# Optimization experiments

Measured on AMD Instinct MI355X. Metric: run time of the kernel, lower is better.

## Reference

```python
import jax, jax.numpy as jnp
import numpy as np

VOCAB, EMBED, HIDDEN = 32000, 256, 512
N, L = 64, 2048

def setup_inputs() -> dict:
    key = jax.random.key(0)
    k1, k2, k3, k4 = jax.random.split(key, 4)
    X = jax.random.randint(k1, (N, L), 0, VOCAB)
    E = jax.random.normal(k2, (VOCAB, EMBED), dtype=jnp.float32) * 0.02
    W_hh = jax.random.normal(k3, (HIDDEN, HIDDEN), dtype=jnp.float32) / np.sqrt(HIDDEN)
    b_hh = jnp.zeros((HIDDEN,), dtype=jnp.float32)
    W_xh = jax.random.normal(k4, (EMBED, HIDDEN), dtype=jnp.float32) / np.sqrt(EMBED)
    b_xh = jnp.zeros((HIDDEN,), dtype=jnp.float32)
    return {"X": X, "E": E, "W_hh": W_hh, "b_hh": b_hh, "W_xh": W_xh, "b_xh": b_xh}

def reference(X, E, W_hh, b_hh, W_xh, b_xh):
    # Embed tokens: (N, L, De)
    xe = E[X]
    # Precompute input projection for all timesteps in one big GEMM: (N, L, H)
    xp = jnp.einsum('nld,dh->nlh', xe, W_xh) + b_xh
    h0 = jnp.zeros((X.shape[0], W_hh.shape[0]), dtype=E.dtype)

    def step(h, x_t):
        # h: (N, H); x_t: (N, H) already projected
        h_new = jnp.tanh(h @ W_hh + b_hh + x_t)
        return h_new, None

    # scan over time: move L to leading axis -> (L, N, H)
    h_last, _ = jax.lax.scan(step, h0, jnp.swapaxes(xp, 0, 1))
    return h_last
```

## Files before the change

kernel.cpp:

```cpp
#include <hip/hip_runtime.h>

typedef _Float16 h8 __attribute__((ext_vector_type(8)));
typedef float f4v __attribute__((ext_vector_type(4)));
typedef unsigned int u32;
typedef unsigned short u16;
typedef unsigned long long u64;
typedef u32 u32x4 __attribute__((ext_vector_type(4)));

#define SEQ 2048
#define HID 512
#define EMB 256
#define NV 32000
#define LOSCALE 2048.0f
#define INV_LOSCALE 4.8828125e-4f

#define WS_WHI 0u
#define WS_WLO (512u * 1024u)
#define WS_HG (1024u * 1024u)
#define WS_FLAGS (WS_HG + 256u * 1024u)
#define WS_PROJ (WS_FLAGS + 4u * 1024u)

__global__ void wsplit_kernel(const float* __restrict__ Whh,
                              _Float16* __restrict__ Whi,
                              _Float16* __restrict__ Wlo) {
  int gid = blockIdx.x * 256 + threadIdx.x;
  int l = gid & 63, c = gid >> 6;
  int kb = c & 15, jtg = c >> 4;
  int j = jtg * 16 + (l & 15);
  int k0 = kb * 32 + (l >> 4) * 8;
  _Float16 hi[8], lo[8];
#pragma unroll
  for (int e = 0; e < 8; ++e) {
    float v = Whh[(k0 + e) * HID + j];
    _Float16 h = (_Float16)v;
    hi[e] = h;
    lo[e] = (_Float16)((v - (float)h) * LOSCALE);
  }
  *(h8*)(Whi + (size_t)gid * 8) = *(const h8*)hi;
  *(h8*)(Wlo + (size_t)gid * 8) = *(const h8*)lo;
}

template <bool PF32>
__global__ __launch_bounds__(256) void proj_kernel(const float* __restrict__ E,
                                                   const float* __restrict__ Wxh,
                                                   const float* __restrict__ bxh,
                                                   void* __restrict__ projE) {
  __shared__ float El[32 * EMB];
  const int t = threadIdx.x;
  const int v0 = blockIdx.x * 32;
  {
    const float4* src = (const float4*)(E + (size_t)v0 * EMB);
    float4* dst = (float4*)El;
#pragma unroll
    for (int i = 0; i < 8; ++i) dst[t + i * 256] = src[t + i * 256];
  }
  __syncthreads();
  const int c0 = (t & 63) * 8;
  const int rg = t >> 6;
  float acc[8][8];
#pragma unroll
  for (int r = 0; r < 8; ++r)
#pragma unroll
    for (int c = 0; c < 8; ++c) acc[r][c] = 0.f;

#pragma unroll 4
  for (int d = 0; d < EMB; ++d) {
    float wv[8];
    *(float4*)&wv[0] = *(const float4*)&Wxh[d * HID + c0];
    *(float4*)&wv[4] = *(const float4*)&Wxh[d * HID + c0 + 4];
#pragma unroll
    for (int r = 0; r < 8; ++r) {
      float ev = El[(rg * 8 + r) * EMB + d];
#pragma unroll
      for (int c = 0; c < 8; ++c) acc[r][c] = fmaf(ev, wv[c], acc[r][c]);
    }
  }
  float bv[8];
  *(float4*)&bv[0] = *(const float4*)&bxh[c0];
  *(float4*)&bv[4] = *(const float4*)&bxh[c0 + 4];
#pragma unroll
  for (int r = 0; r < 8; ++r) {
    int row = v0 + rg * 8 + r;
    if (PF32) {
      float o[8];
#pragma unroll
      for (int c = 0; c < 8; ++c) o[c] = acc[r][c] + bv[c];
      *(float4*)((float*)projE + (size_t)row * HID + c0) = *(const float4*)&o[0];
      *(float4*)((float*)projE + (size_t)row * HID + c0 + 4) = *(const float4*)&o[4];
    } else {
      _Float16 o[8];
#pragma unroll
      for (int c = 0; c < 8; ++c) o[c] = (_Float16)(acc[r][c] + bv[c]);
      *(h8*)((_Float16*)projE + (size_t)row * HID + c0) = *(const h8*)o;
    }
  }
}

__global__ void init_kernel(float4* __restrict__ p) {
  int gid = blockIdx.x * 256 + threadIdx.x;
  if (gid < 16640) {
    float4 z = {0.f, 0.f, 0.f, 0.f};
    if (gid >= 8192 && gid < 16384) {
      float one = __uint_as_float(1u);
      z = (float4){one, one, one, one};
    }
    p[gid] = z;
  }
}

template <bool PF32>
__global__ __launch_bounds__(512, 2) void rnn_kernel(
    const int* __restrict__ X, const _Float16* __restrict__ Whi,
    const _Float16* __restrict__ Wlo, const void* __restrict__ projE,
    const float* __restrict__ bhh, u32* __restrict__ hX,
    float* __restrict__ out) {
  __shared__ u32 hs[8192];
  const int tid = threadIdx.x;
  const int w = tid >> 6, lane = tid & 63;
  const int g = lane >> 4, li = lane & 15;
  const int grp = blockIdx.x >> 2, cb = blockIdx.x & 3;
  const int nb = grp * 16;
  const int jtg = cb * 8 + w;
  const int j = jtg * 16 + li;

  h8 Wh[16], Wl[16];
  {
    const char* wb = (const char*)Whi + ((size_t)jtg * 16 * 64 + lane) * 16;
    const char* wb2 = (const char*)Wlo + ((size_t)jtg * 16 * 64 + lane) * 16;
#pragma unroll
    for (int kb = 0; kb < 16; ++kb) {
      Wh[kb] = *(const h8*)(wb + (size_t)kb * 1024);
      Wl[kb] = *(const h8*)(wb2 + (size_t)kb * 1024);
    }
#pragma unroll
    for (int kb = 0; kb < 16; ++kb) {
      f4v th = __builtin_bit_cast(f4v, Wh[kb]);
      f4v tl = __builtin_bit_cast(f4v, Wl[kb]);
      asm volatile("" : "+v"(th), "+v"(tl));
      Wh[kb] = __builtin_bit_cast(h8, th);
      Wl[kb] = __builtin_bit_cast(h8, tl);
    }
  }
  const float bias = bhh[j];

  const int hi2 = ((jtg & 1) << 1) | (li >> 3);
  const int pub0 = (li & 1) * 4096 + (jtg >> 1) * 256 + (hi2 << 6) + g * 16 +
                   ((li & 7) >> 1);
  u32* const hgrp = hX + grp * 8192;
  const bool oddli = (li & 1) != 0;

  const int* Xr[4];
#pragma unroll
  for (int i = 0; i < 4; ++i) Xr[i] = X + (size_t)(nb + g * 4 + i) * SEQ;

  for (int t = 0; t < SEQ; ++t) {
    float pv[4];
#pragma unroll
    for (int i = 0; i < 4; ++i) {
      int tok = Xr[i][t];
      if (PF32)
        pv[i] = ((const float*)projE)[(size_t)tok * HID + j];
      else
        pv[i] = (float)((const _Float16*)projE)[(size_t)tok * HID + j];
    }

    const u32 e = (u32)(t >> 1) & 1u;
    const u32* src = hgrp + (t & 1) * 32768 + tid * 4;
    u64 v[4][2];
    {
      int tries = 0;
      while (true) {
#pragma unroll
        for (int q = 0; q < 4; ++q) {
          v[q][0] = __hip_atomic_load((const u64*)(src + q * 2048),
                                      __ATOMIC_RELAXED,
                                      __HIP_MEMORY_SCOPE_AGENT);
          v[q][1] = __hip_atomic_load((const u64*)(src + q * 2048 + 2),
                                      __ATOMIC_RELAXED,
                                      __HIP_MEMORY_SCOPE_AGENT);
        }
        u64 orr = (v[0][0] | v[0][1]) | (v[1][0] | v[1][1]) |
                  (v[2][0] | v[2][1]) | (v[3][0] | v[3][1]);
        u64 andd = (v[0][0] & v[0][1]) & (v[1][0] & v[1][1]) &
                   (v[2][0] & v[2][1]) & (v[3][0] & v[3][1]);
        bool ok;
        if (e)
          ok = ((andd & 1ull) != 0) && (((andd >> 32) & 1ull) != 0);
        else
          ok = ((orr & 1ull) == 0) && (((orr >> 32) & 1ull) == 0);
        if (__all(ok) || ++tries > 200000) break;
      }
    }
#pragma unroll
    for (int q = 0; q < 4; ++q) {
      u32x4 d;
      d[0] = (u32)v[q][0]; d[1] = (u32)(v[q][0] >> 32);
      d[2] = (u32)v[q][1]; d[3] = (u32)(v[q][1] >> 32);
      *(u32x4*)(hs + tid * 4 + q * 2048) = d;
    }
    __syncthreads();

    f4v a1 = {0.f, 0.f, 0.f, 0.f};
    f4v c1 = {0.f, 0.f, 0.f, 0.f};
    f4v c2 = {0.f, 0.f, 0.f, 0.f};
    const u32* hb_hi = hs + lane * 4;
    const u32* hb_lo = hb_hi + 4096;
#pragma unroll
    for (int kb = 0; kb < 16; ++kb) {
      h8 ahc = *(const h8*)(hb_hi + kb * 256);
      h8 alc = *(const h8*)(hb_lo + kb * 256);
      a1 = __builtin_amdgcn_mfma_f32_16x16x32_f16(ahc, Wh[kb], a1, 0, 0, 0);
      c1 = __builtin_amdgcn_mfma_f32_16x16x32_f16(ahc, Wl[kb], c1, 0, 0, 0);
      c2 = __builtin_amdgcn_mfma_f32_16x16x32_f16(alc, Wh[kb], c2, 0, 0, 0);
    }

    u32* const hn = hgrp + ((t + 1) & 1) * 32768;
    const u32 ep = (u32)((t + 1) >> 1) & 1u;
    const bool lastt = (t == SEQ - 1);
#pragma unroll
    for (int i = 0; i < 4; ++i) {
      float vfull = a1[i] + INV_LOSCALE * (c1[i] + c2[i]) + bias + pv[i];
      float e2 = __expf(2.0f * vfull);
      float th = 1.0f - 2.0f / (e2 + 1.0f);
      _Float16 hh = (_Float16)th;
      u16 h16 = __builtin_bit_cast(u16, hh);
      if (!oddli) h16 = (u16)((h16 & 0xFFFEu) | ep);
      hh = __builtin_bit_cast(_Float16, h16);
      _Float16 hl = (_Float16)((th - (float)hh) * LOSCALE);
      u16 l16 = __builtin_bit_cast(u16, hl);
      if (!oddli) l16 = (u16)((l16 & 0xFFFEu) | ep);
      u32 pk = (u32)h16 | ((u32)l16 << 16);
      u32 nbv = (u32)__shfl_xor((int)pk, 1, 64);
      u32 word = oddli ? ((nbv >> 16) | (pk & 0xFFFF0000u))
                       : ((pk & 0xFFFFu) | (nbv << 16));
      __hip_atomic_store(hn + pub0 + i * 4, word, __ATOMIC_RELAXED,
                         __HIP_MEMORY_SCOPE_AGENT);
      if (lastt) out[(nb + g * 4 + i) * HID + j] = th;
    }
    __syncthreads();
  }
}

extern "C" void kernel_launch(void* const* d_in, const int* in_sizes, int n_in,
                              void* d_out, int out_size, void* d_ws,
                              size_t ws_size, hipStream_t stream) {
  const int* X = (const int*)d_in[0];
  const float* E = (const float*)d_in[1];
  const float* Whh = (const float*)d_in[2];
  const float* bhh = (const float*)d_in[3];
  const float* Wxh = (const float*)d_in[4];
  const float* bxh = (const float*)d_in[5];
  float* out = (float*)d_out;

  char* ws = (char*)d_ws;
  _Float16* Whi = (_Float16*)(ws + WS_WHI);
  _Float16* Wlo = (_Float16*)(ws + WS_WLO);
  u32* hX = (u32*)(ws + WS_HG);
  void* projE = (void*)(ws + WS_PROJ);
  const bool pf32 = ws_size >= (size_t)WS_PROJ + (size_t)NV * HID * sizeof(float);

  wsplit_kernel<<<128, 256, 0, stream>>>(Whh, Whi, Wlo);
  init_kernel<<<65, 256, 0, stream>>>((float4*)(ws + WS_HG));
  if (pf32) {
    proj_kernel<true><<<NV / 32, 256, 0, stream>>>(E, Wxh, bxh, projE);
    rnn_kernel<true><<<16, 512, 0, stream>>>(X, Whi, Wlo, projE, bhh, hX, out);
  } else {
    proj_kernel<false><<<NV / 32, 256, 0, stream>>>(E, Wxh, bxh, projE);
    rnn_kernel<false><<<16, 512, 0, stream>>>(X, Whi, Wlo, projE, bhh, hX, out);
  }
}
```

Before: 6.453 ms.

## Co-locate each RNN block group on one XCD and use sc0 loads for exchange

The RNN kernel now launches 64 blocks. Each block reads its hardware XCC ID and atomically claims a slot, so each group of four cooperating blocks lands on the same XCD. Surplus blocks exit. When all four blocks of a group confirm they can see each other's sc0 (XCD-local L2) stores, the hidden-state exchange switches to sc0 global loads and stores instead of agent-scope atomics, which cuts per-step cross-XCD coherence latency. The cost is a startup claim-and-handshake phase, reliance on the claim region being zeroed by init, and dependence on hardware-specific cache coherence behaviour.

```diff
diff --git a/kernel.cpp b/kernel.cpp
--- a/kernel.cpp
+++ b/kernel.cpp
@@ -17,8 +17,58 @@
 #define WS_WHI 0u
 #define WS_WLO (512u * 1024u)
 #define WS_HG (1024u * 1024u)
-#define WS_FLAGS (WS_HG + 256u * 1024u)
-#define WS_PROJ (WS_FLAGS + 4u * 1024u)
+#define WS_CLAIM (WS_HG + 256u * 1024u)
+#define WS_PROJ (WS_CLAIM + 4u * 1024u)
+
+static __device__ __forceinline__ u32 ld_sc0_u32(const u32* p) {
+  u32 r;
+  asm volatile("global_load_dword %0, %1, off sc0\n\ts_waitcnt vmcnt(0)"
+               : "=v"(r) : "v"(p) : "memory");
+  return r;
+}
+static __device__ __forceinline__ void st_sc0_u32(u32* p, u32 v) {
+  asm volatile("global_store_dword %0, %1, off sc0" ::"v"(p), "v"(v)
+               : "memory");
+}
+
+template <bool SC0>
+static __device__ __forceinline__ void load8(const u32* src, u64 v[4][2]) {
+  if constexpr (SC0) {
+    asm volatile(
+        "global_load_dwordx2 %0, %8, off sc0\n\t"
+        "global_load_dwordx2 %1, %9, off sc0\n\t"
+        "global_load_dwordx2 %2, %10, off sc0\n\t"
+        "global_load_dwordx2 %3, %11, off sc0\n\t"
+        "global_load_dwordx2 %4, %12, off sc0\n\t"
+        "global_load_dwordx2 %5, %13, off sc0\n\t"
+        "global_load_dwordx2 %6, %14, off sc0\n\t"
+        "global_load_dwordx2 %7, %15, off sc0\n\t"
+        "s_waitcnt vmcnt(0)"
+        : "=&v"(v[0][0]), "=&v"(v[0][1]), "=&v"(v[1][0]), "=&v"(v[1][1]),
+          "=&v"(v[2][0]), "=&v"(v[2][1]), "=&v"(v[3][0]), "=&v"(v[3][1])
+        : "v"((const u64*)(src)), "v"((const u64*)(src + 2)),
+          "v"((const u64*)(src + 2048)), "v"((const u64*)(src + 2050)),
+          "v"((const u64*)(src + 4096)), "v"((const u64*)(src + 4098)),
+          "v"((const u64*)(src + 6144)), "v"((const u64*)(src + 6146))
+        : "memory");
+  } else {
+#pragma unroll
+    for (int q = 0; q < 4; ++q) {
+      v[q][0] = __hip_atomic_load((const u64*)(src + q * 2048),
+                                  __ATOMIC_RELAXED, __HIP_MEMORY_SCOPE_AGENT);
+      v[q][1] = __hip_atomic_load((const u64*)(src + q * 2048 + 2),
+                                  __ATOMIC_RELAXED, __HIP_MEMORY_SCOPE_AGENT);
+    }
+  }
+}
+template <bool SC0>
+static __device__ __forceinline__ void st_ex(u32* p, u32 v) {
+  if constexpr (SC0)
+    asm volatile("global_store_dword %0, %1, off sc0" ::"v"(p), "v"(v)
+                 : "memory");
+  else
+    __hip_atomic_store(p, v, __ATOMIC_RELAXED, __HIP_MEMORY_SCOPE_AGENT);
+}
 
 __global__ void wsplit_kernel(const float* __restrict__ Whh,
                               _Float16* __restrict__ Whi,
@@ -108,17 +158,14 @@
   }
 }
 
-template <bool PF32>
-__global__ __launch_bounds__(512, 2) void rnn_kernel(
+template <bool PF32, bool SC0>
+static __device__ __forceinline__ void rnn_loop(
     const int* __restrict__ X, const _Float16* __restrict__ Whi,
     const _Float16* __restrict__ Wlo, const void* __restrict__ projE,
     const float* __restrict__ bhh, u32* __restrict__ hX,
-    float* __restrict__ out) {
-  __shared__ u32 hs[8192];
-  const int tid = threadIdx.x;
+    float* __restrict__ out, u32* hs, int tid, int grp, int cb) {
   const int w = tid >> 6, lane = tid & 63;
   const int g = lane >> 4, li = lane & 15;
-  const int grp = blockIdx.x >> 2, cb = blockIdx.x & 3;
   const int nb = grp * 16;
   const int jtg = cb * 8 + w;
   const int j = jtg * 16 + li;
@@ -170,15 +217,7 @@
     {
       int tries = 0;
       while (true) {
-#pragma unroll
-        for (int q = 0; q < 4; ++q) {
-          v[q][0] = __hip_atomic_load((const u64*)(src + q * 2048),
-                                      __ATOMIC_RELAXED,
-                                      __HIP_MEMORY_SCOPE_AGENT);
-          v[q][1] = __hip_atomic_load((const u64*)(src + q * 2048 + 2),
-                                      __ATOMIC_RELAXED,
-                                      __HIP_MEMORY_SCOPE_AGENT);
-        }
+        load8<SC0>(src, v);
         u64 orr = (v[0][0] | v[0][1]) | (v[1][0] | v[1][1]) |
                   (v[2][0] | v[2][1]) | (v[3][0] | v[3][1]);
         u64 andd = (v[0][0] & v[0][1]) & (v[1][0] & v[1][1]) &
@@ -233,12 +272,98 @@
       u32 nbv = (u32)__shfl_xor((int)pk, 1, 64);
       u32 word = oddli ? ((nbv >> 16) | (pk & 0xFFFF0000u))
                        : ((pk & 0xFFFFu) | (nbv << 16));
-      __hip_atomic_store(hn + pub0 + i * 4, word, __ATOMIC_RELAXED,
-                         __HIP_MEMORY_SCOPE_AGENT);
+      st_ex<SC0>(hn + pub0 + i * 4, word);
       if (lastt) out[(nb + g * 4 + i) * HID + j] = th;
     }
     __syncthreads();
   }
+}
+
+template <bool PF32>
+__global__ __launch_bounds__(512, 2) void rnn_kernel(
+    const int* __restrict__ X, const _Float16* __restrict__ Whi,
+    const _Float16* __restrict__ Wlo, const void* __restrict__ projE,
+    const float* __restrict__ bhh, u32* __restrict__ hX,
+    u32* __restrict__ claim, float* __restrict__ out) {
+  __shared__ u32 hs[8192];
+  __shared__ int sh[3];
+  const int tid = threadIdx.x;
+
+  if (tid == 0) {
+    u32 xcd;
+    asm volatile("s_getreg_b32 %0, hwreg(HW_REG_XCC_ID)" : "=s"(xcd));
+    xcd &= 7u;
+    int mygrp = -1, mycb = 0;
+    u32 slot = __hip_atomic_fetch_add(claim + xcd * 32, 1u, __ATOMIC_RELAXED,
+                                      __HIP_MEMORY_SCOPE_AGENT);
+    u32 quad = slot >> 2, pos = slot & 3;
+    if (quad < 16u) {
+      u32* qg = claim + 512 + xcd * 16 + quad;
+      if (pos == 3) {
+        u32 g = __hip_atomic_fetch_add(claim + 256, 1u, __ATOMIC_RELAXED,
+                                       __HIP_MEMORY_SCOPE_AGENT);
+        __hip_atomic_store(qg, (g < 4u) ? (g + 1u) : 255u, __ATOMIC_RELAXED,
+                           __HIP_MEMORY_SCOPE_AGENT);
+        if (g < 4u) mygrp = (int)g;
+      } else {
+        long grace = -1;
+        for (u32 it = 0;; ++it) {
+          u32 qv = __hip_atomic_load(qg, __ATOMIC_RELAXED,
+                                     __HIP_MEMORY_SCOPE_AGENT);
+          if (qv) {
+            if (qv <= 4u) mygrp = (int)qv - 1;
+            break;
+          }
+          u32 gc = __hip_atomic_load(claim + 256, __ATOMIC_RELAXED,
+                                     __HIP_MEMORY_SCOPE_AGENT);
+          if (gc >= 4u) {
+            if (grace < 0) grace = (long)it + 30000;
+            else if ((long)it > grace) break;
+          }
+          if (it > 200000u) break;
+        }
+      }
+      mycb = (int)pos;
+    }
+    sh[0] = mygrp;
+    sh[1] = mycb;
+  }
+  __syncthreads();
+  const int grp = sh[0], cb = sh[1];
+  if (grp < 0) return;
+
+  if (tid == 0) {
+    u32* ht = claim + 640 + grp * 16;
+    st_sc0_u32(ht + cb * 4, 1u);
+    int seen = 0;
+    for (u32 it = 0; it < 300u && seen < 4; ++it) {
+      seen = 0;
+#pragma unroll
+      for (int b = 0; b < 4; ++b) seen += (ld_sc0_u32(ht + b * 4) == 1u);
+    }
+    u32* vd = claim + 768 + grp * 16;
+    __hip_atomic_store(vd + cb * 4, (seen == 4) ? 2u : 1u, __ATOMIC_RELAXED,
+                       __HIP_MEMORY_SCOPE_AGENT);
+    u32 all = 2u;
+#pragma unroll
+    for (int b = 0; b < 4; ++b) {
+      u32 vv = 0;
+      for (u32 it = 0; it < 10000u; ++it) {
+        vv = __hip_atomic_load(vd + b * 4, __ATOMIC_RELAXED,
+                               __HIP_MEMORY_SCOPE_AGENT);
+        if (vv) break;
+      }
+      if (vv != 2u) all = 1u;
+    }
+    sh[2] = (all == 2u) ? 1 : 0;
+  }
+  __syncthreads();
+  const bool usesc0 = sh[2] != 0;
+
+  if (usesc0)
+    rnn_loop<PF32, true>(X, Whi, Wlo, projE, bhh, hX, out, hs, tid, grp, cb);
+  else
+    rnn_loop<PF32, false>(X, Whi, Wlo, projE, bhh, hX, out, hs, tid, grp, cb);
 }
 
 extern "C" void kernel_launch(void* const* d_in, const int* in_sizes, int n_in,
@@ -256,6 +381,7 @@
   _Float16* Whi = (_Float16*)(ws + WS_WHI);
   _Float16* Wlo = (_Float16*)(ws + WS_WLO);
   u32* hX = (u32*)(ws + WS_HG);
+  u32* claim = (u32*)(ws + WS_CLAIM);
   void* projE = (void*)(ws + WS_PROJ);
   const bool pf32 = ws_size >= (size_t)WS_PROJ + (size_t)NV * HID * sizeof(float);
 
@@ -263,9 +389,11 @@
   init_kernel<<<65, 256, 0, stream>>>((float4*)(ws + WS_HG));
   if (pf32) {
     proj_kernel<true><<<NV / 32, 256, 0, stream>>>(E, Wxh, bxh, projE);
-    rnn_kernel<true><<<16, 512, 0, stream>>>(X, Whi, Wlo, projE, bhh, hX, out);
+    rnn_kernel<true><<<64, 512, 0, stream>>>(X, Whi, Wlo, projE, bhh, hX,
+                                             claim, out);
   } else {
     proj_kernel<false><<<NV / 32, 256, 0, stream>>>(E, Wxh, bxh, projE);
-    rnn_kernel<false><<<16, 512, 0, stream>>>(X, Whi, Wlo, projE, bhh, hX, out);
-  }
-}
+    rnn_kernel<false><<<64, 512, 0, stream>>>(X, Whi, Wlo, projE, bhh, hX,
+                                              claim, out);
+  }
+}
```

New measurement: 6.059 ms. -6.1%, faster.
